# Kernel tuning notes

Measured on AMD Instinct MI355X. Metric: run time of the kernel, lower is better.

## Reference

```python
import jax, jax.numpy as jnp
import numpy as np

D_MODEL = 1024
N_HEADS = 16
D_K = D_MODEL // N_HEADS
D_FF = 4096
LN_EPS = 1e-5


def _layer_norm(x, gamma, beta):
    mu = jnp.mean(x, axis=-1, keepdims=True)
    var = jnp.mean(jnp.square(x - mu), axis=-1, keepdims=True)
    return (x - mu) * jax.lax.rsqrt(var + LN_EPS) * gamma + beta


def setup_inputs() -> dict:
    key = jax.random.key(0)
    ks = jax.random.split(key, 16)
    B, S = 2, 2048
    x = jax.random.normal(ks[0], (B, S, D_MODEL), dtype=jnp.float32)
    # causal mask: True = masked (as used by masked_fill)
    mask = ~jnp.tril(jnp.ones((S, S), dtype=bool))
    s = 1.0 / np.sqrt(D_MODEL)
    sf = 1.0 / np.sqrt(D_FF)
    inp = {
        "x": x,
        "mask": mask,
        "ln1_g": jnp.ones((D_MODEL,), jnp.float32),
        "ln1_b": jnp.zeros((D_MODEL,), jnp.float32),
        "ln2_g": jnp.ones((D_MODEL,), jnp.float32),
        "ln2_b": jnp.zeros((D_MODEL,), jnp.float32),
        "Wq": jax.random.normal(ks[1], (D_MODEL, D_MODEL), jnp.float32) * s,
        "bq": jax.random.normal(ks[2], (D_MODEL,), jnp.float32) * s,
        "Wk": jax.random.normal(ks[3], (D_MODEL, D_MODEL), jnp.float32) * s,
        "bk": jax.random.normal(ks[4], (D_MODEL,), jnp.float32) * s,
        "Wv": jax.random.normal(ks[5], (D_MODEL, D_MODEL), jnp.float32) * s,
        "bv": jax.random.normal(ks[6], (D_MODEL,), jnp.float32) * s,
        "Wo": jax.random.normal(ks[7], (D_MODEL, D_MODEL), jnp.float32) * s,
        "bo": jax.random.normal(ks[8], (D_MODEL,), jnp.float32) * s,
        "W1": jax.random.normal(ks[9], (D_MODEL, D_FF), jnp.float32) * s,
        "b1": jax.random.normal(ks[10], (D_FF,), jnp.float32) * s,
        "W2": jax.random.normal(ks[11], (D_FF, D_MODEL), jnp.float32) * sf,
        "b2": jax.random.normal(ks[12], (D_MODEL,), jnp.float32) * sf,
    }
    return inp


def reference(x, mask, ln1_g, ln1_b, ln2_g, ln2_b,
              Wq, bq, Wk, bk, Wv, bv, Wo, bo, W1, b1, W2, b2):
    B, S, _ = x.shape
    normed = _layer_norm(x, ln1_g, ln1_b)
    # project and split heads: [B, H, S, Dk]
    def split_heads(t):
        return t.reshape(B, S, N_HEADS, D_K).transpose(0, 2, 1, 3)
    Q = split_heads(normed @ Wq + bq)
    K = split_heads(normed @ Wk + bk)
    V = split_heads(normed @ Wv + bv)
    qk = jnp.einsum("bhsd,bhtd->bhst", Q, K)  # [B, H, S, S]
    qk = jnp.where(mask, -jnp.inf, qk)  # mask applied BEFORE scaling, as in source
    attn = jax.nn.softmax(qk / np.sqrt(D_K), axis=-1)
    attn_out = jnp.einsum("bhst,bhtd->bhsd", attn, V)
    attn_out = attn_out.transpose(0, 2, 1, 3).reshape(B, S, D_MODEL)
    attn_out = attn_out @ Wo + bo
    res = attn_out + x  # dropout_p=0 (eval)
    h = _layer_norm(res, ln2_g, ln2_b)
    h = jax.nn.gelu(h @ W1 + b1, approximate=False)
    h = h @ W2 + b2
    return res + h
```

## Files before the change

### kernel.cpp

```cpp
#include <hip/hip_runtime.h>


typedef __bf16 bf16;
typedef __bf16 bf16x8 __attribute__((ext_vector_type(8)));
typedef float f32x4 __attribute__((ext_vector_type(4)));

#define NROWS 4096
#define DM 1024
#define SEQ 2048
#define NHEAD 16
#define DKH 64
#define DFF 4096
#define QSCALE 0.18033688f

#define GLL16(gptr, lptr) \
  __builtin_amdgcn_global_load_lds((const __attribute__((address_space(1))) void*)(gptr), \
                                   (__attribute__((address_space(3))) void*)(lptr), 16, 0, 0)

static char* g_scratch = nullptr;
namespace {
struct ScratchInit {
  ScratchInit() {
    void* p = nullptr;
    if (hipMalloc(&p, (size_t)128 * 1024 * 1024) == hipSuccess) g_scratch = (char*)p;
  }
};
static ScratchInit g_scratch_init;
}

__global__ __launch_bounds__(256) void ln_kernel(const float* __restrict__ inp,
                                                 const float* __restrict__ gamma,
                                                 const float* __restrict__ beta,
                                                 bf16* __restrict__ out) {
  int row = blockIdx.x;
  int t = threadIdx.x;
  float4 xv = *((const float4*)(inp + (size_t)row * DM) + t);
  float v[4] = {xv.x, xv.y, xv.z, xv.w};
  float s = 0.f, sq = 0.f;
#pragma unroll
  for (int i = 0; i < 4; i++) { s += v[i]; sq += v[i] * v[i]; }
#pragma unroll
  for (int m = 32; m >= 1; m >>= 1) { s += __shfl_xor(s, m); sq += __shfl_xor(sq, m); }
  __shared__ float rs[4], rq[4];
  int w = t >> 6, lane = t & 63;
  if (lane == 0) { rs[w] = s; rq[w] = sq; }
  __syncthreads();
  s = rs[0] + rs[1] + rs[2] + rs[3];
  sq = rq[0] + rq[1] + rq[2] + rq[3];
  float mu = s * (1.f / DM);
  float var = sq * (1.f / DM) - mu * mu;
  float rinv = rsqrtf(var + 1e-5f);
  float4 gv = *((const float4*)gamma + t);
  float4 bv = *((const float4*)beta + t);
  float g[4] = {gv.x, gv.y, gv.z, gv.w}, b[4] = {bv.x, bv.y, bv.z, bv.w};
  bf16 ov[4];
#pragma unroll
  for (int i = 0; i < 4; i++) ov[i] = (bf16)((v[i] - mu) * rinv * g[i] + b[i]);
  *(uint2*)(out + (size_t)row * DM + t * 4) = *(uint2*)ov;
}

__global__ __launch_bounds__(256) void concat_bias(const float* __restrict__ bq,
                                                   const float* __restrict__ bk,
                                                   const float* __restrict__ bv,
                                                   float* __restrict__ cat) {
  int i = blockIdx.x * 256 + threadIdx.x;
  float v = (i < 1024) ? bq[i] : (i < 2048 ? bk[i - 1024] : bv[i - 2048]);
  cat[i] = v;
}

__global__ __launch_bounds__(1024) void transpose_f32_bf16(const float* __restrict__ in,
                                                           bf16* __restrict__ out,
                                                           int R, int C) {
  __shared__ bf16 tile[32][33];
  int x = blockIdx.x * 32 + threadIdx.x;
  int y = blockIdx.y * 32 + threadIdx.y;
  tile[threadIdx.y][threadIdx.x] = (bf16)in[(size_t)y * C + x];
  __syncthreads();
  int ox = blockIdx.y * 32 + threadIdx.x;
  int oy = blockIdx.x * 32 + threadIdx.y;
  out[(size_t)oy * R + ox] = tile[threadIdx.x][threadIdx.y];
}

__global__ __launch_bounds__(1024) void transpose_bf16(const bf16* __restrict__ in,
                                                       bf16* __restrict__ out,
                                                       int R, int C) {
  __shared__ bf16 tile[32][33];
  size_t zoff = (size_t)blockIdx.z * (size_t)R * (size_t)C;
  int x = blockIdx.x * 32 + threadIdx.x;
  int y = blockIdx.y * 32 + threadIdx.y;
  tile[threadIdx.y][threadIdx.x] = in[zoff + (size_t)y * C + x];
  __syncthreads();
  int ox = blockIdx.y * 32 + threadIdx.x;
  int oy = blockIdx.x * 32 + threadIdx.y;
  out[zoff + (size_t)oy * R + ox] = tile[threadIdx.x][threadIdx.y];
}

#define BM 128
#define BK 64

#define EPI_QKV3 0
#define EPI_ATTN_RES 1
#define EPI_GELU 2
#define EPI_FFN2 3

template<int EPI, int BNT>
__global__ __launch_bounds__(256, 2) void gemm_bt(
    const bf16* __restrict__ A, const bf16* __restrict__ Bt,
    const float* __restrict__ bias, int Kd, int N,
    bf16* __restrict__ outb, float* __restrict__ outf,
    const float* __restrict__ add) {
  constexpr int MS = (BNT == 128) ? 4 : 2;
  __shared__ bf16 As[BM * BK];
  __shared__ bf16 Bs[BNT * BK];
  int t = threadIdx.x;
  int m0 = blockIdx.y * BM, n0 = blockIdx.x * BNT;
  int w = t >> 6, lane = t & 63, ln = lane & 15, quad = lane >> 4;
  int wm = (BNT == 128) ? (w >> 1) * 64 : w * 32;
  int wn = (BNT == 128) ? (w & 1) * 64 : 0;
  f32x4 acc[MS][4];
#pragma unroll
  for (int i = 0; i < MS; i++)
#pragma unroll
    for (int j = 0; j < 4; j++) acc[i][j] = (f32x4){0.f, 0.f, 0.f, 0.f};

  int lr = (t >> 3) & 7, lc = t & 7;
  int gcol = ((lc ^ lr) * 8);
  const bf16* Ab = A + (size_t)(m0 + w * 8 + lr) * Kd + gcol;
  const bf16* Bb = Bt + (size_t)(n0 + w * 8 + lr) * Kd + gcol;
  bf16* AsW = As + (w * 8) * BK;
  bf16* BsW = Bs + (w * 8) * BK;

  for (int k0 = 0; k0 < Kd; k0 += BK) {
    __syncthreads();
#pragma unroll
    for (int j = 0; j < 4; j++)
      GLL16(Ab + (size_t)(32 * j) * Kd + k0, AsW + 32 * j * BK);
#pragma unroll
    for (int j = 0; j < BNT / 32; j++)
      GLL16(Bb + (size_t)(32 * j) * Kd + k0, BsW + 32 * j * BK);
    __syncthreads();
#pragma unroll
    for (int kk = 0; kk < 2; kk++) {
      bf16x8 af[MS], bfr[4];
#pragma unroll
      for (int ms = 0; ms < MS; ms++) {
        int r = wm + ms * 16 + ln;
        af[ms] = *(const bf16x8*)(As + r * BK + (((kk * 4 + quad) ^ (r & 7)) * 8));
      }
#pragma unroll
      for (int ns = 0; ns < 4; ns++) {
        int r = wn + ns * 16 + ln;
        bfr[ns] = *(const bf16x8*)(Bs + r * BK + (((kk * 4 + quad) ^ (r & 7)) * 8));
      }
#pragma unroll
      for (int ms = 0; ms < MS; ms++)
#pragma unroll
        for (int ns = 0; ns < 4; ns++)
          acc[ms][ns] = __builtin_amdgcn_mfma_f32_16x16x32_bf16(af[ms], bfr[ns], acc[ms][ns], 0, 0, 0);
    }
  }

#pragma unroll
  for (int ms = 0; ms < MS; ms++) {
#pragma unroll
    for (int ns = 0; ns < 4; ns++) {
      int col = n0 + wn + ns * 16 + ln;
      float bv = bias[col];
#pragma unroll
      for (int r = 0; r < 4; r++) {
        int row = m0 + wm + ms * 16 + quad * 4 + r;
        float val = acc[ms][ns][r] + bv;
        if (EPI == EPI_QKV3) {
          int which = col >> 10, cc = col & 1023;
          int h = cc >> 6, dk = cc & 63;
          float sc = (which == 0) ? QSCALE : 1.f;
          int b = row >> 11, sx = row & 2047;
          outb[(size_t)which * (4 << 20) +
               ((((size_t)b * NHEAD + h) * SEQ) + sx) * DKH + dk] = (bf16)(val * sc);
        } else if (EPI == EPI_ATTN_RES) {
          size_t idx = (size_t)row * DM + col;
          outf[idx] = val + add[idx];
        } else if (EPI == EPI_GELU) {
          float gl = 0.5f * val * (1.f + erff(val * 0.7071067811865475f));
          outb[(size_t)row * N + col] = (bf16)gl;
        } else {
          size_t idx = (size_t)row * DM + col;
          outf[idx] = val + add[idx];
        }
      }
    }
  }
}

#define LSTR 72
#define OSTR 68

__global__ __launch_bounds__(256) void attn_kernel(
    const bf16* __restrict__ Q, const bf16* __restrict__ K,
    const bf16* __restrict__ Vt, bf16* __restrict__ out) {
  __shared__ float smem[4608];
  int lin = blockIdx.x;
  int bh = lin & 31;
  int qq = 63 - (lin >> 5);
  int t = threadIdx.x, w = t >> 6, lane = t & 63, ln = lane & 15, quad = lane >> 4;
  int qbase = qq * 32;
  size_t bhS = (size_t)bh * SEQ;
  const bf16* Vg0 = Vt + (size_t)bh * DKH * SEQ;
  bf16* Pw = (bf16*)smem + w * 32 * LSTR;

  bf16x8 qa[2][2];
#pragma unroll
  for (int m = 0; m < 2; m++)
#pragma unroll
    for (int ks = 0; ks < 2; ks++)
      qa[m][ks] = *(const bf16x8*)(Q + (bhS + qbase + m * 16 + ln) * DKH + ks * 32 + quad * 8);

  bf16x8 ones;
#pragma unroll
  for (int i = 0; i < 8; i++) ones[i] = (bf16)1.0f;

  f32x4 o[2][4];
#pragma unroll
  for (int m = 0; m < 2; m++)
#pragma unroll
    for (int i = 0; i < 4; i++) o[m][i] = (f32x4){0.f, 0.f, 0.f, 0.f};
  f32x4 accl[2] = {(f32x4){0.f, 0.f, 0.f, 0.f}, (f32x4){0.f, 0.f, 0.f, 0.f}};

  int ktmax = qq >> 1;
  for (int kt = w; kt <= ktmax; kt += 4) {
    const bf16* Kg = K + (bhS + kt * 64) * DKH;
    bf16x8 kbf[8], vbf[8];
#pragma unroll
    for (int ns = 0; ns < 4; ns++)
#pragma unroll
      for (int ks = 0; ks < 2; ks++)
        kbf[ns * 2 + ks] = *(const bf16x8*)(Kg + (ns * 16 + ln) * DKH + ks * 32 + quad * 8);
#pragma unroll
    for (int ns = 0; ns < 4; ns++)
#pragma unroll
      for (int ks = 0; ks < 2; ks++)
        vbf[ns * 2 + ks] = *(const bf16x8*)(Vg0 + (size_t)(ns * 16 + ln) * SEQ + kt * 64 + ks * 32 + quad * 8);

    f32x4 s[2][4];
#pragma unroll
    for (int m = 0; m < 2; m++)
#pragma unroll
      for (int ns = 0; ns < 4; ns++) s[m][ns] = (f32x4){0.f, 0.f, 0.f, 0.f};
#pragma unroll
    for (int ns = 0; ns < 4; ns++)
#pragma unroll
      for (int m = 0; m < 2; m++) {
        s[m][ns] = __builtin_amdgcn_mfma_f32_16x16x32_bf16(qa[m][0], kbf[ns * 2], s[m][ns], 0, 0, 0);
        s[m][ns] = __builtin_amdgcn_mfma_f32_16x16x32_bf16(qa[m][1], kbf[ns * 2 + 1], s[m][ns], 0, 0, 0);
      }
    if (kt == ktmax) {
#pragma unroll
      for (int m = 0; m < 2; m++)
#pragma unroll
        for (int ns = 0; ns < 4; ns++)
#pragma unroll
          for (int r = 0; r < 4; r++) {
            int qrow = qbase + m * 16 + quad * 4 + r;
            int kpos = kt * 64 + ns * 16 + ln;
            if (kpos > qrow) s[m][ns][r] = -30000.f;
          }
    }
#pragma unroll
    for (int m = 0; m < 2; m++)
#pragma unroll
      for (int ns = 0; ns < 4; ns++)
#pragma unroll
        for (int r = 0; r < 4; r++)
          Pw[(m * 16 + quad * 4 + r) * LSTR + ns * 16 + ln] =
              (bf16)__builtin_amdgcn_exp2f(s[m][ns][r]);
    bf16x8 pa[2][2];
#pragma unroll
    for (int m = 0; m < 2; m++) {
      pa[m][0] = *(const bf16x8*)(Pw + (m * 16 + ln) * LSTR + quad * 8);
      pa[m][1] = *(const bf16x8*)(Pw + (m * 16 + ln) * LSTR + 32 + quad * 8);
    }
#pragma unroll
    for (int m = 0; m < 2; m++) {
      accl[m] = __builtin_amdgcn_mfma_f32_16x16x32_bf16(pa[m][0], ones, accl[m], 0, 0, 0);
      accl[m] = __builtin_amdgcn_mfma_f32_16x16x32_bf16(pa[m][1], ones, accl[m], 0, 0, 0);
    }
#pragma unroll
    for (int ns2 = 0; ns2 < 4; ns2++)
#pragma unroll
      for (int m = 0; m < 2; m++) {
        o[m][ns2] = __builtin_amdgcn_mfma_f32_16x16x32_bf16(pa[m][0], vbf[ns2 * 2], o[m][ns2], 0, 0, 0);
        o[m][ns2] = __builtin_amdgcn_mfma_f32_16x16x32_bf16(pa[m][1], vbf[ns2 * 2 + 1], o[m][ns2], 0, 0, 0);
      }
  }

  float* Ob = smem;
  float* Lb = smem + 2 * 32 * OSTR;
  __syncthreads();
#pragma unroll
  for (int m = 0; m < 2; m++) {
    if (w < 2) {
#pragma unroll
      for (int ns2 = 0; ns2 < 4; ns2++)
#pragma unroll
        for (int r = 0; r < 4; r++)
          Ob[(w * 32 + m * 16 + quad * 4 + r) * OSTR + ns2 * 16 + ln] = o[m][ns2][r];
    }
    if (ln == 0) {
#pragma unroll
      for (int r = 0; r < 4; r++) Lb[w * 32 + m * 16 + quad * 4 + r] = accl[m][r];
    }
  }
  __syncthreads();
  if (w >= 2) {
#pragma unroll
    for (int m = 0; m < 2; m++)
#pragma unroll
      for (int ns2 = 0; ns2 < 4; ns2++)
#pragma unroll
        for (int r = 0; r < 4; r++) {
          int idx = ((w - 2) * 32 + m * 16 + quad * 4 + r) * OSTR + ns2 * 16 + ln;
          Ob[idx] += o[m][ns2][r];
        }
  }
  __syncthreads();

  int r = t >> 3, c0 = (t & 7) * 8;
  float l = Lb[r] + Lb[32 + r] + Lb[64 + r] + Lb[96 + r];
  float inv = 1.f / l;
  bf16 ov[8];
#pragma unroll
  for (int j = 0; j < 8; j++) {
    float v = Ob[r * OSTR + c0 + j] + Ob[(32 + r) * OSTR + c0 + j];
    ov[j] = (bf16)(v * inv);
  }
  int b = bh >> 4, h = bh & 15;
  *(uint4*)(out + ((size_t)b * SEQ + qbase + r) * DM + h * DKH + c0) = *(uint4*)ov;
}

extern "C" void kernel_launch(void* const* d_in, const int* in_sizes, int n_in,
                              void* d_out, int out_size, void* d_ws, size_t ws_size,
                              hipStream_t stream) {
  const float* x    = (const float*)d_in[0];
  const float* ln1g = (const float*)d_in[2];
  const float* ln1b = (const float*)d_in[3];
  const float* ln2g = (const float*)d_in[4];
  const float* ln2b = (const float*)d_in[5];
  const float* Wq = (const float*)d_in[6];   const float* bq = (const float*)d_in[7];
  const float* Wk = (const float*)d_in[8];   const float* bk = (const float*)d_in[9];
  const float* Wv = (const float*)d_in[10];  const float* bv = (const float*)d_in[11];
  const float* Wo = (const float*)d_in[12];  const float* bo = (const float*)d_in[13];
  const float* W1 = (const float*)d_in[14];  const float* b1 = (const float*)d_in[15];
  const float* W2 = (const float*)d_in[16];  const float* b2 = (const float*)d_in[17];
  float* outp = (float*)d_out;

  char* scratch = g_scratch ? g_scratch : (char*)d_ws;

  bf16* Wqt = (bf16*)scratch;
  bf16* Wkt = Wqt + (1 << 20);
  bf16* Wvt = Wkt + (1 << 20);
  bf16* Wot = Wvt + (1 << 20);
  bf16* W1t = Wot + (1 << 20);
  bf16* W2t = W1t + (4 << 20);
  bf16* normed = W2t + (4 << 20);
  bf16* Qb = normed + (4 << 20);
  bf16* Kb = Qb + (4 << 20);
  bf16* Vb = Kb + (4 << 20);
  bf16* Vtb = Vb + (4 << 20);
  bf16* attn_o = Vtb + (4 << 20);
  float* resf = (float*)(attn_o + (4 << 20));
  float* bias_cat = resf + (4 << 20);
  bf16* h1 = Qb;

  dim3 b256(256), b1k(32, 32);

  ln_kernel<<<NROWS, b256, 0, stream>>>(x, ln1g, ln1b, normed);
  concat_bias<<<12, b256, 0, stream>>>(bq, bk, bv, bias_cat);

  transpose_f32_bf16<<<dim3(32, 32), b1k, 0, stream>>>(Wq, Wqt, 1024, 1024);
  transpose_f32_bf16<<<dim3(32, 32), b1k, 0, stream>>>(Wk, Wkt, 1024, 1024);
  transpose_f32_bf16<<<dim3(32, 32), b1k, 0, stream>>>(Wv, Wvt, 1024, 1024);
  transpose_f32_bf16<<<dim3(32, 32), b1k, 0, stream>>>(Wo, Wot, 1024, 1024);
  transpose_f32_bf16<<<dim3(128, 32), b1k, 0, stream>>>(W1, W1t, 1024, 4096);
  transpose_f32_bf16<<<dim3(32, 128), b1k, 0, stream>>>(W2, W2t, 4096, 1024);

  gemm_bt<EPI_QKV3, 128><<<dim3(24, 32), b256, 0, stream>>>(
      normed, Wqt, bias_cat, 1024, 3072, Qb, nullptr, nullptr);

  transpose_bf16<<<dim3(2, 64, 32), b1k, 0, stream>>>(Vb, Vtb, 2048, 64);

  attn_kernel<<<dim3(2048), b256, 0, stream>>>(Qb, Kb, Vtb, attn_o);

  gemm_bt<EPI_ATTN_RES, 64><<<dim3(16, 32), b256, 0, stream>>>(
      attn_o, Wot, bo, 1024, 1024, nullptr, resf, x);

  ln_kernel<<<NROWS, b256, 0, stream>>>(resf, ln2g, ln2b, normed);

  gemm_bt<EPI_GELU, 128><<<dim3(32, 32), b256, 0, stream>>>(
      normed, W1t, b1, 1024, 4096, h1, nullptr, nullptr);

  gemm_bt<EPI_FFN2, 64><<<dim3(16, 32), b256, 0, stream>>>(
      h1, W2t, b2, 4096, 1024, nullptr, outp, resf);
}
```

Before: 389.2 us.

## Load GEMM operands directly from global into registers with double buffering

The GEMM kernel no longer stages A and B tiles in LDS through global_load_lds. Each wave now loads its MFMA fragments straight from global memory into registers, using a two-stage register double buffer to overlap loads with MFMA work. This removes LDS traffic and the block-wide barriers, but operands shared between waves are no longer reused through LDS, so global/L2 traffic rises and each lane does strided 16-byte loads. Register pressure also grows under launch_bounds(256,2).

```diff
diff --git a/kernel.cpp b/kernel.cpp
--- a/kernel.cpp
+++ b/kernel.cpp
@@ -12,10 +12,6 @@
 #define DKH 64
 #define DFF 4096
 #define QSCALE 0.18033688f
-
-#define GLL16(gptr, lptr) \
-  __builtin_amdgcn_global_load_lds((const __attribute__((address_space(1))) void*)(gptr), \
-                                   (__attribute__((address_space(3))) void*)(lptr), 16, 0, 0)
 
 static char* g_scratch = nullptr;
 namespace {
@@ -96,7 +92,6 @@
 }
 
 #define BM 128
-#define BK 64
 
 #define EPI_QKV3 0
 #define EPI_ATTN_RES 1
@@ -110,8 +105,6 @@
     bf16* __restrict__ outb, float* __restrict__ outf,
     const float* __restrict__ add) {
   constexpr int MS = (BNT == 128) ? 4 : 2;
-  __shared__ bf16 As[BM * BK];
-  __shared__ bf16 Bs[BNT * BK];
   int t = threadIdx.x;
   int m0 = blockIdx.y * BM, n0 = blockIdx.x * BNT;
   int w = t >> 6, lane = t & 63, ln = lane & 15, quad = lane >> 4;
@@ -123,42 +116,47 @@
 #pragma unroll
     for (int j = 0; j < 4; j++) acc[i][j] = (f32x4){0.f, 0.f, 0.f, 0.f};
 
-  int lr = (t >> 3) & 7, lc = t & 7;
-  int gcol = ((lc ^ lr) * 8);
-  const bf16* Ab = A + (size_t)(m0 + w * 8 + lr) * Kd + gcol;
-  const bf16* Bb = Bt + (size_t)(n0 + w * 8 + lr) * Kd + gcol;
-  bf16* AsW = As + (w * 8) * BK;
-  bf16* BsW = Bs + (w * 8) * BK;
-
-  for (int k0 = 0; k0 < Kd; k0 += BK) {
-    __syncthreads();
-#pragma unroll
-    for (int j = 0; j < 4; j++)
-      GLL16(Ab + (size_t)(32 * j) * Kd + k0, AsW + 32 * j * BK);
-#pragma unroll
-    for (int j = 0; j < BNT / 32; j++)
-      GLL16(Bb + (size_t)(32 * j) * Kd + k0, BsW + 32 * j * BK);
-    __syncthreads();
-#pragma unroll
-    for (int kk = 0; kk < 2; kk++) {
-      bf16x8 af[MS], bfr[4];
-#pragma unroll
-      for (int ms = 0; ms < MS; ms++) {
-        int r = wm + ms * 16 + ln;
-        af[ms] = *(const bf16x8*)(As + r * BK + (((kk * 4 + quad) ^ (r & 7)) * 8));
-      }
-#pragma unroll
-      for (int ns = 0; ns < 4; ns++) {
-        int r = wn + ns * 16 + ln;
-        bfr[ns] = *(const bf16x8*)(Bs + r * BK + (((kk * 4 + quad) ^ (r & 7)) * 8));
-      }
-#pragma unroll
-      for (int ms = 0; ms < MS; ms++)
-#pragma unroll
-        for (int ns = 0; ns < 4; ns++)
-          acc[ms][ns] = __builtin_amdgcn_mfma_f32_16x16x32_bf16(af[ms], bfr[ns], acc[ms][ns], 0, 0, 0);
-    }
-  }
+  const bf16* Ab = A + (size_t)(m0 + wm + ln) * Kd + quad * 8;
+  const bf16* Bb = Bt + (size_t)(n0 + wn + ln) * Kd + quad * 8;
+
+  bf16x8 a0[MS][2], b0[4][2], a1[MS][2], b1[4][2];
+
+#define LOAD_A(dst, k)                                                        \
+  {                                                                           \
+    _Pragma("unroll") for (int ms = 0; ms < MS; ms++)                         \
+        _Pragma("unroll") for (int ks = 0; ks < 2; ks++)                      \
+            dst[ms][ks] = *(const bf16x8*)(Ab + (size_t)(ms * 16) * Kd + (k) + ks * 32); \
+  }
+#define LOAD_B(dst, k)                                                        \
+  {                                                                           \
+    _Pragma("unroll") for (int ns = 0; ns < 4; ns++)                          \
+        _Pragma("unroll") for (int ks = 0; ks < 2; ks++)                      \
+            dst[ns][ks] = *(const bf16x8*)(Bb + (size_t)(ns * 16) * Kd + (k) + ks * 32); \
+  }
+#define MFMA_STEP(af, bf)                                                     \
+  {                                                                           \
+    _Pragma("unroll") for (int ms = 0; ms < MS; ms++)                         \
+        _Pragma("unroll") for (int ns = 0; ns < 4; ns++)                      \
+            _Pragma("unroll") for (int ks = 0; ks < 2; ks++)                  \
+                acc[ms][ns] = __builtin_amdgcn_mfma_f32_16x16x32_bf16(        \
+                    af[ms][ks], bf[ns][ks], acc[ms][ns], 0, 0, 0);            \
+  }
+
+  LOAD_A(a0, 0);
+  LOAD_B(b0, 0);
+  for (int k0 = 0; k0 < Kd; k0 += 128) {
+    LOAD_A(a1, k0 + 64);
+    LOAD_B(b1, k0 + 64);
+    MFMA_STEP(a0, b0);
+    if (k0 + 128 < Kd) {
+      LOAD_A(a0, k0 + 128);
+      LOAD_B(b0, k0 + 128);
+    }
+    MFMA_STEP(a1, b1);
+  }
+#undef LOAD_A
+#undef LOAD_B
+#undef MFMA_STEP
 
 #pragma unroll
   for (int ms = 0; ms < MS; ms++) {
```

Result: slower. 692.0 us (+77.8%).

## Stage GEMM epilogue through LDS for vectorized stores and use fast GELU

Applied to the files above, without the earlier changes.

The GEMM epilogue now writes biased accumulators into per-wave LDS tiles, then each lane reads back 32 contiguous values and emits 16-byte vector stores (and vector residual loads). This replaces scattered per-element global stores that caused poorly coalesced writes. GELU switches from erff to an exp2/rcp sigmoid-form tanh approximation, cutting transcendental cost while introducing a small approximation error versus exact GELU. LDS usage grows to fit the staging buffer.

```diff
diff --git a/kernel.cpp b/kernel.cpp
--- a/kernel.cpp
+++ b/kernel.cpp
@@ -97,6 +97,7 @@
 
 #define BM 128
 #define BK 64
+#define ESTR 68
 
 #define EPI_QKV3 0
 #define EPI_ATTN_RES 1
@@ -110,8 +111,9 @@
     bf16* __restrict__ outb, float* __restrict__ outf,
     const float* __restrict__ add) {
   constexpr int MS = (BNT == 128) ? 4 : 2;
-  __shared__ bf16 As[BM * BK];
-  __shared__ bf16 Bs[BNT * BK];
+  __shared__ __align__(16) char smem[34816];
+  bf16* As = (bf16*)smem;
+  bf16* Bs = As + BM * BK;
   int t = threadIdx.x;
   int m0 = blockIdx.y * BM, n0 = blockIdx.x * BNT;
   int w = t >> 6, lane = t & 63, ln = lane & 15, quad = lane >> 4;
@@ -124,9 +126,9 @@
     for (int j = 0; j < 4; j++) acc[i][j] = (f32x4){0.f, 0.f, 0.f, 0.f};
 
   int lr = (t >> 3) & 7, lc = t & 7;
-  int gcol = ((lc ^ lr) * 8);
-  const bf16* Ab = A + (size_t)(m0 + w * 8 + lr) * Kd + gcol;
-  const bf16* Bb = Bt + (size_t)(n0 + w * 8 + lr) * Kd + gcol;
+  int gcolsw = ((lc ^ lr) * 8);
+  const bf16* Ab = A + (size_t)(m0 + w * 8 + lr) * Kd + gcolsw;
+  const bf16* Bb = Bt + (size_t)(n0 + w * 8 + lr) * Kd + gcolsw;
   bf16* AsW = As + (w * 8) * BK;
   bf16* BsW = Bs + (w * 8) * BK;
 
@@ -160,33 +162,64 @@
     }
   }
 
-#pragma unroll
-  for (int ms = 0; ms < MS; ms++) {
-#pragma unroll
-    for (int ns = 0; ns < 4; ns++) {
-      int col = n0 + wn + ns * 16 + ln;
-      float bv = bias[col];
-#pragma unroll
-      for (int r = 0; r < 4; r++) {
-        int row = m0 + wm + ms * 16 + quad * 4 + r;
-        float val = acc[ms][ns][r] + bv;
-        if (EPI == EPI_QKV3) {
-          int which = col >> 10, cc = col & 1023;
-          int h = cc >> 6, dk = cc & 63;
-          float sc = (which == 0) ? QSCALE : 1.f;
-          int b = row >> 11, sx = row & 2047;
-          outb[(size_t)which * (4 << 20) +
-               ((((size_t)b * NHEAD + h) * SEQ) + sx) * DKH + dk] = (bf16)(val * sc);
-        } else if (EPI == EPI_ATTN_RES) {
-          size_t idx = (size_t)row * DM + col;
-          outf[idx] = val + add[idx];
-        } else if (EPI == EPI_GELU) {
-          float gl = 0.5f * val * (1.f + erff(val * 0.7071067811865475f));
-          outb[(size_t)row * N + col] = (bf16)gl;
-        } else {
-          size_t idx = (size_t)row * DM + col;
-          outf[idx] = val + add[idx];
-        }
+  __syncthreads();
+  float* Ew = (float*)smem + w * (32 * ESTR);
+  int erow = lane >> 1;
+  int ec0 = (lane & 1) * 32;
+  constexpr int HALVES = (BNT == 128) ? 2 : 1;
+#pragma unroll
+  for (int half = 0; half < HALVES; half++) {
+#pragma unroll
+    for (int msl = 0; msl < 2; msl++) {
+      int ms = half * 2 + msl;
+#pragma unroll
+      for (int ns = 0; ns < 4; ns++) {
+        float bv = bias[n0 + wn + ns * 16 + ln];
+#pragma unroll
+        for (int r = 0; r < 4; r++)
+          Ew[(msl * 16 + quad * 4 + r) * ESTR + ns * 16 + ln] = acc[ms][ns][r] + bv;
+      }
+    }
+    int grow = m0 + wm + half * 32 + erow;
+    int gcol = n0 + wn + ec0;
+    float v[32];
+#pragma unroll
+    for (int j = 0; j < 8; j++) {
+      float4 tv = *(const float4*)(Ew + erow * ESTR + ec0 + j * 4);
+      v[j * 4 + 0] = tv.x; v[j * 4 + 1] = tv.y; v[j * 4 + 2] = tv.z; v[j * 4 + 3] = tv.w;
+    }
+    if (EPI == EPI_QKV3) {
+      int which = gcol >> 10, cc = gcol & 1023;
+      int h = cc >> 6, dk0 = cc & 63;
+      float sc = (which == 0) ? QSCALE : 1.f;
+      int b = grow >> 11, sx = grow & 2047;
+      bf16 ov[32];
+#pragma unroll
+      for (int j = 0; j < 32; j++) ov[j] = (bf16)(v[j] * sc);
+      bf16* dst = outb + (size_t)which * (4 << 20) +
+                  ((((size_t)b * NHEAD + h) * SEQ) + sx) * DKH + dk0;
+#pragma unroll
+      for (int j = 0; j < 4; j++) *(uint4*)(dst + j * 8) = *(uint4*)(ov + j * 8);
+    } else if (EPI == EPI_GELU) {
+      bf16 ov[32];
+#pragma unroll
+      for (int j = 0; j < 32; j++) {
+        float x = v[j];
+        float u = __builtin_amdgcn_exp2f(x * fmaf(0.102944f, x * x, 2.3021204f));
+        ov[j] = (bf16)(x * u * __builtin_amdgcn_rcpf(1.f + u));
+      }
+      bf16* dst = outb + (size_t)grow * N + gcol;
+#pragma unroll
+      for (int j = 0; j < 4; j++) *(uint4*)(dst + j * 8) = *(uint4*)(ov + j * 8);
+    } else {
+      const float* ap = add + (size_t)grow * DM + gcol;
+      float* op = outf + (size_t)grow * DM + gcol;
+#pragma unroll
+      for (int j = 0; j < 8; j++) {
+        float4 av = *(const float4*)(ap + j * 4);
+        float4 o4 = {v[j * 4 + 0] + av.x, v[j * 4 + 1] + av.y,
+                     v[j * 4 + 2] + av.z, v[j * 4 + 3] + av.w};
+        *(float4*)(op + j * 4) = o4;
       }
     }
   }
```

New measurement: 401.5 us. 3.1% more time.
